# Kernel optimization log

Hardware: AMD Instinct MI355X
Metric: run time of the kernel (lower is better)

## Reference

```python
import jax, jax.numpy as jnp
import numpy as np

N_AUDIO = 32768  # n_audio_samples


def upsample_linear(x, out_size):
    """torch F.interpolate(mode='linear', align_corners=False) along last axis."""
    t = x.shape[-1]
    pos = (jnp.arange(out_size, dtype=x.dtype) + 0.5) * (t / out_size) - 0.5
    pos = jnp.clip(pos, 0.0, t - 1)
    i0 = jnp.floor(pos).astype(jnp.int32)
    i1 = jnp.minimum(i0 + 1, t - 1)
    w = pos - i0.astype(x.dtype)
    return jnp.take(x, i0, axis=-1) * (1.0 - w) + jnp.take(x, i1, axis=-1) * w


def setup_inputs() -> dict:
    key = jax.random.key(0)
    k1, k2, k3, k4, k5 = jax.random.split(key, 5)
    B, C, T, N_OSC = 8, 128, 128, 128
    x = jax.random.normal(k1, (B, C, T), dtype=jnp.float32)
    # conv1d kernel_size=1 weights -> plain [out, in] matrices + bias
    amp_w = jax.random.normal(k2, (N_OSC, C), dtype=jnp.float32) * 0.08
    amp_b = jax.random.normal(k3, (N_OSC,), dtype=jnp.float32) * 0.08
    freq_w = jax.random.normal(k4, (N_OSC, C), dtype=jnp.float32) * 0.08
    freq_b = jax.random.normal(k5, (N_OSC,), dtype=jnp.float32) * 0.08
    return {"x": x, "amp_w": amp_w, "amp_b": amp_b, "freq_w": freq_w, "freq_b": freq_b}


def reference(x, amp_w, amp_b, freq_w, freq_b):
    # 1x1 conv == per-frame matmul: [B,C,T] x [O,C] -> [B,O,T]
    amp = jax.nn.sigmoid(jnp.einsum('bct,oc->bot', x, amp_w) + amp_b[None, :, None])
    freq = jax.nn.sigmoid(jnp.einsum('bct,oc->bot', x, freq_w) + freq_b[None, :, None])
    # upsample control signals to audio rate: [B,O,T] -> [B,O,N_AUDIO]
    amp = upsample_linear(amp, N_AUDIO)
    freq = upsample_linear(freq, N_AUDIO)
    # additive synthesis: cumulative phase -> sin -> amp -> mean over oscillators
    phase = jnp.cumsum(freq * jnp.pi, axis=-1)
    audio = jnp.sin(phase) * amp
    return jnp.mean(audio, axis=1, keepdims=True)  # [B,1,N_AUDIO]
```

## Files before the change

### kernel.cpp

```cpp
#include <hip/hip_runtime.h>
#include <hip/hip_bf16.h>
#include <math.h>

#define N_AUDIO 32768
#define NB 8
#define NC 128
#define NT 128
#define NO 128


__global__ __launch_bounds__(128)
void prep_kernel(const float* __restrict__ x,
                 const float* __restrict__ amp_w,
                 const float* __restrict__ amp_b,
                 const float* __restrict__ freq_w,
                 const float* __restrict__ freq_b,
                 float4* __restrict__ SEG,
                 float*  __restrict__ CW)
{
    const int bo = blockIdx.x;
    const int b  = bo >> 7;
    const int o  = bo & 127;
    const int t  = threadIdx.x;

    const float* xp = x + b * (NC * NT) + t;
    const float* wa = amp_w  + o * NC;
    const float* wf = freq_w + o * NC;

    float va = 0.f, vf = 0.f;
#pragma unroll 8
    for (int c = 0; c < NC; ++c) {
        float xv = xp[c * NT];
        va = fmaf(xv, wa[c], va);
        vf = fmaf(xv, wf[c], vf);
    }
    va += amp_b[o];
    vf += freq_b[o];
    const float sa = 1.f / (1.f + __expf(-va));
    const float sf = 1.f / (1.f + __expf(-vf));

    __shared__ float  fsh[NT];
    __shared__ float  ash[NT];
    __shared__ double psh[NT];
    fsh[t] = sf;
    ash[t] = sa;
    psh[t] = (double)sf;
    __syncthreads();

    for (int off = 1; off < NT; off <<= 1) {
        double add = (t >= off) ? psh[t - off] : 0.0;
        double v   = psh[t];
        __syncthreads();
        psh[t] = v + add;
        __syncthreads();
    }
    const double incl = psh[t];
    const double excl = incl - (double)sf;
    double Cd = 128.0 * excl + 64.0 * (double)sf;
    Cd -= floor(Cd);

    const float df = (t < NT - 1) ? (fsh[t + 1] - sf) : 0.f;
    const float da = (t < NT - 1) ? (ash[t + 1] - sa) : 0.f;

    const int idx = (b * NT + t) * NO + o;
    SEG[idx] = make_float4(0.5f * sf,
                           df * (1.f / 1024.f),
                           sa * (1.f / 128.f),
                           da * (1.f / 128.f));
    CW[idx]  = (float)Cd;
}

__global__ __launch_bounds__(128)
void synth_kernel(const float4* __restrict__ SEG,
                  const float*  __restrict__ CW,
                  float* __restrict__ out)
{
    const int c   = blockIdx.x;
    const int b   = blockIdx.y;
    const int tid = threadIdx.x;

    int row; float m, mask;
    if (c == 0) { row = 0;            m = (float)(tid - 127); mask = 0.f; }
    else if (c & 1) { row = (c - 1) >> 1; m = (float)(tid + 1);   mask = 1.f; }
    else        { row = (c >> 1) - 1; m = (float)(tid + 129); mask = 1.f; }

    const float m2 = m * m * mask;
    const float wA = (m - 0.5f) * (1.f / 256.f) * mask;

    const float4* __restrict__ P = SEG + (b * NT + row) * NO;
    const float*  __restrict__ C = CW  + (b * NT + row) * NO;

    float sum0 = 0.f, sum1 = 0.f;
#pragma unroll 4
    for (int o = 0; o < NO; o += 2) {
        const float4 p0 = P[o];
        const float4 p1 = P[o + 1];
        const float  c0 = C[o];
        const float  c1 = C[o + 1];
        const float z0 = fmaf(m2, p0.y, fmaf(m, p0.x, c0));
        const float z1 = fmaf(m2, p1.y, fmaf(m, p1.x, c1));
        const float a0 = fmaf(wA, p0.w, p0.z);
        const float a1 = fmaf(wA, p1.w, p1.z);
        sum0 = fmaf(a0, __builtin_amdgcn_sinf(__builtin_amdgcn_fractf(z0)), sum0);
        sum1 = fmaf(a1, __builtin_amdgcn_sinf(__builtin_amdgcn_fractf(z1)), sum1);
    }
    out[b * N_AUDIO + c * 128 + tid] = sum0 + sum1;
}

extern "C" void kernel_launch(void* const* d_in, const int* in_sizes, int n_in,
                              void* d_out, int out_size, void* d_ws, size_t ws_size,
                              hipStream_t stream)
{
    const float* x      = (const float*)d_in[0];
    const float* amp_w  = (const float*)d_in[1];
    const float* amp_b  = (const float*)d_in[2];
    const float* freq_w = (const float*)d_in[3];
    const float* freq_b = (const float*)d_in[4];
    float* out = (float*)d_out;

    float4* SEG = (float4*)d_ws;
    float*  CW  = (float*)((char*)d_ws + (size_t)NB * NT * NO * sizeof(float4));

    prep_kernel<<<dim3(NB * NO), dim3(128), 0, stream>>>(
        x, amp_w, amp_b, freq_w, freq_b, SEG, CW);
    synth_kernel<<<dim3(N_AUDIO / 128, NB), dim3(128), 0, stream>>>(SEG, CW, out);
}
```

Before: 84.60 us.

## Stage segment coefficients in LDS and compute four samples per thread

The synth kernel is restructured so each wavefront handles one whole 256-sample segment row (or the head task). Each lane computes four output samples and reuses one set of per-oscillator coefficients, which are staged once into shared memory. This cuts repeated global loads of the segment coefficients and gives more independent sin/FMA chains per thread. In exchange the grid shrinks to 33x8 blocks, which may leave compute units underused, and some wavefronts exit idle after loading.

```diff
diff --git a/kernel.cpp b/kernel.cpp
--- a/kernel.cpp
+++ b/kernel.cpp
@@ -70,41 +70,82 @@
     CW[idx]  = (float)Cd;
 }
 
-__global__ __launch_bounds__(128)
+__global__ __launch_bounds__(256)
 void synth_kernel(const float4* __restrict__ SEG,
                   const float*  __restrict__ CW,
                   float* __restrict__ out)
 {
-    const int c   = blockIdx.x;
-    const int b   = blockIdx.y;
-    const int tid = threadIdx.x;
+    const int b    = blockIdx.y;
+    const int tid  = threadIdx.x;
+    const int w    = tid >> 6;
+    const int l    = tid & 63;
+    const int task = blockIdx.x * 4 + w;
 
-    int row; float m, mask;
-    if (c == 0) { row = 0;            m = (float)(tid - 127); mask = 0.f; }
-    else if (c & 1) { row = (c - 1) >> 1; m = (float)(tid + 1);   mask = 1.f; }
-    else        { row = (c >> 1) - 1; m = (float)(tid + 129); mask = 1.f; }
+    __shared__ __align__(16) float4 sP[4][NO];
+    __shared__ __align__(16) float  sC[4][NO];
 
-    const float m2 = m * m * mask;
-    const float wA = (m - 0.5f) * (1.f / 256.f) * mask;
+    const int isHead = (task >= 128) ? 1 : 0;
+    const int row    = isHead ? 0 : task;
+    const int base   = (b * NT + row) * NO;
 
-    const float4* __restrict__ P = SEG + (b * NT + row) * NO;
-    const float*  __restrict__ C = CW  + (b * NT + row) * NO;
+    sP[w][l]      = SEG[base + l];
+    sP[w][l + 64] = SEG[base + l + 64];
+    sC[w][l]      = CW[base + l];
+    sC[w][l + 64] = CW[base + l + 64];
+    __syncthreads();
 
-    float sum0 = 0.f, sum1 = 0.f;
+    if (task > 128) return;
+
+    const float mask  = isHead ? 0.f : 1.f;
+    const float mofs  = isHead ? -127.f : 1.f;
+    const int   jbase = isHead ? 0 : 256 * row + 128;
+
+    float mm[4], m2[4], wA[4];
+#pragma unroll
+    for (int jj = 0; jj < 4; ++jj) {
+        const float m = (float)(l + 64 * jj) + mofs;
+        mm[jj] = m;
+        m2[jj] = m * m * mask;
+        wA[jj] = (m - 0.5f) * (1.f / 256.f) * mask;
+    }
+
+    float accE[4] = {0.f, 0.f, 0.f, 0.f};
+    float accO[4] = {0.f, 0.f, 0.f, 0.f};
+
+    const float4* __restrict__ P = sP[w];
+    const float*  __restrict__ C = sC[w];
+
 #pragma unroll 4
-    for (int o = 0; o < NO; o += 2) {
-        const float4 p0 = P[o];
+    for (int o = 0; o < NO; o += 4) {
+        const float4 p0 = P[o + 0];
         const float4 p1 = P[o + 1];
-        const float  c0 = C[o];
-        const float  c1 = C[o + 1];
-        const float z0 = fmaf(m2, p0.y, fmaf(m, p0.x, c0));
-        const float z1 = fmaf(m2, p1.y, fmaf(m, p1.x, c1));
-        const float a0 = fmaf(wA, p0.w, p0.z);
-        const float a1 = fmaf(wA, p1.w, p1.z);
-        sum0 = fmaf(a0, __builtin_amdgcn_sinf(__builtin_amdgcn_fractf(z0)), sum0);
-        sum1 = fmaf(a1, __builtin_amdgcn_sinf(__builtin_amdgcn_fractf(z1)), sum1);
+        const float4 p2 = P[o + 2];
+        const float4 p3 = P[o + 3];
+        const float4 c4 = *reinterpret_cast<const float4*>(&C[o]);
+#pragma unroll
+        for (int jj = 0; jj < 4; ++jj) {
+            const float z0 = fmaf(m2[jj], p0.y, fmaf(mm[jj], p0.x, c4.x));
+            const float z1 = fmaf(m2[jj], p1.y, fmaf(mm[jj], p1.x, c4.y));
+            const float z2 = fmaf(m2[jj], p2.y, fmaf(mm[jj], p2.x, c4.z));
+            const float z3 = fmaf(m2[jj], p3.y, fmaf(mm[jj], p3.x, c4.w));
+            const float a0 = fmaf(wA[jj], p0.w, p0.z);
+            const float a1 = fmaf(wA[jj], p1.w, p1.z);
+            const float a2 = fmaf(wA[jj], p2.w, p2.z);
+            const float a3 = fmaf(wA[jj], p3.w, p3.z);
+            accE[jj] = fmaf(a0, __builtin_amdgcn_sinf(__builtin_amdgcn_fractf(z0)), accE[jj]);
+            accO[jj] = fmaf(a1, __builtin_amdgcn_sinf(__builtin_amdgcn_fractf(z1)), accO[jj]);
+            accE[jj] = fmaf(a2, __builtin_amdgcn_sinf(__builtin_amdgcn_fractf(z2)), accE[jj]);
+            accO[jj] = fmaf(a3, __builtin_amdgcn_sinf(__builtin_amdgcn_fractf(z3)), accO[jj]);
+        }
     }
-    out[b * N_AUDIO + c * 128 + tid] = sum0 + sum1;
+
+#pragma unroll
+    for (int jj = 0; jj < 4; ++jj) {
+        const int s  = l + 64 * jj;
+        const int js = jbase + s;
+        const bool valid = isHead ? (s < 128) : (js < N_AUDIO);
+        if (valid) out[b * N_AUDIO + js] = accE[jj] + accO[jj];
+    }
 }
 
 extern "C" void kernel_launch(void* const* d_in, const int* in_sizes, int n_in,
@@ -123,5 +164,5 @@
 
     prep_kernel<<<dim3(NB * NO), dim3(128), 0, stream>>>(
         x, amp_w, amp_b, freq_w, freq_b, SEG, CW);
-    synth_kernel<<<dim3(N_AUDIO / 128, NB), dim3(128), 0, stream>>>(SEG, CW, out);
+    synth_kernel<<<dim3(33, NB), dim3(256), 0, stream>>>(SEG, CW, out);
 }
```

New measurement: 84.54 us. Within noise of the previous version (-0.1%).
